# Kernel tuning notes

Measured on AMD Instinct MI355X. Metric: run time of the kernel, lower is better.

Reference implementation:

```python
import jax, jax.numpy as jnp
import numpy as np

N = 4096      # num_nodes
B = 32        # batch
U = 64        # num_units
L = 2         # num_rnn_layers
K = 2         # max_diffusion_step
OUT = 1       # output_dim (also decoder input_dim)
NM = 2 * K + 1  # num_matrices: 2 supports * K cheb steps + identity


def _random_walk_T(adj):
    # calculate_random_walk_matrix(adj).T : (D^-1 W)^T
    d = adj.sum(axis=1)
    return (adj / d[:, None]).T


def setup_inputs():
    key = jax.random.key(0)
    ks = jax.random.split(key, 16)
    adj = jax.random.uniform(ks[0], (N, N), dtype=jnp.float32)
    S_fwd = _random_walk_T(adj)      # forward transition, transposed
    S_bwd = _random_walk_T(adj.T)    # backward transition, transposed

    inputs = jax.random.normal(ks[1], (B, N, OUT), dtype=jnp.float32)
    hidden_state = jax.random.normal(ks[2], (L, B, N, U), dtype=jnp.float32) * 0.1

    D0 = OUT + U   # layer 0 gconv input width
    D1 = U + U     # layer 1 gconv input width
    s = 0.05
    Wg0 = jax.random.normal(ks[3], (NM * D0, 2 * U), jnp.float32) * s
    bg0 = jnp.ones((2 * U,), jnp.float32)          # bias_start = 1.0 for gates
    Wc0 = jax.random.normal(ks[4], (NM * D0, U), jnp.float32) * s
    bc0 = jnp.zeros((U,), jnp.float32)
    Wg1 = jax.random.normal(ks[5], (NM * D1, 2 * U), jnp.float32) * s
    bg1 = jnp.ones((2 * U,), jnp.float32)
    Wc1 = jax.random.normal(ks[6], (NM * D1, U), jnp.float32) * s
    bc1 = jnp.zeros((U,), jnp.float32)
    Wp = jax.random.normal(ks[7], (U, OUT), jnp.float32) * s
    bp = jnp.zeros((OUT,), jnp.float32)
    return {
        "inputs": inputs, "hidden_state": hidden_state,
        "S_fwd": S_fwd, "S_bwd": S_bwd,
        "Wg0": Wg0, "bg0": bg0, "Wc0": Wc0, "bc0": bc0,
        "Wg1": Wg1, "bg1": bg1, "Wc1": Wc1, "bc1": bc1,
        "Wp": Wp, "bp": bp,
    }


def _gconv(supports, x, h, W, b):
    # diffusion graph convolution with Chebyshev recursion (DCRNN)
    x0 = jnp.concatenate([x, h], axis=-1)      # (B, N, D)
    xs = [x0]
    for S in supports:
        x1 = jnp.einsum('mn,bnd->bmd', S, x0)
        xs.append(x1)
        xk_2, xk_1 = x0, x1
        for _ in range(K - 1):
            x2 = 2.0 * jnp.einsum('mn,bnd->bmd', S, xk_1) - xk_2
            xs.append(x2)
            xk_2, xk_1 = xk_1, x2
    X = jnp.concatenate(xs, axis=-1)           # (B, N, NM*D)
    return X @ W + b


def _dcgru_cell(supports, x, h, Wg, bg, Wc, bc):
    value = jax.nn.sigmoid(_gconv(supports, x, h, Wg, bg))   # (B, N, 2U)
    r, u = jnp.split(value, 2, axis=-1)
    c = jnp.tanh(_gconv(supports, x, r * h, Wc, bc))
    return u * h + (1.0 - u) * c


def reference(inputs, hidden_state, S_fwd, S_bwd,
              Wg0, bg0, Wc0, bc0, Wg1, bg1, Wc1, bc1, Wp, bp):
    supports = (S_fwd, S_bwd)
    layer_params = [(Wg0, bg0, Wc0, bc0), (Wg1, bg1, Wc1, bc1)]
    out = inputs
    new_hidden = []
    for i, (Wg, bg, Wc, bc) in enumerate(layer_params):
        h = _dcgru_cell(supports, out, hidden_state[i], Wg, bg, Wc, bc)
        new_hidden.append(h)
        out = h
    predict = out @ Wp + bp                    # (B, N, OUT)
    return predict, jnp.stack(new_hidden)
```

## Files before the change

kernel.cpp:

```cpp
#include <hip/hip_runtime.h>

typedef unsigned short u16;
typedef unsigned int u32;
typedef unsigned long long u64;
typedef short v8s __attribute__((ext_vector_type(8)));
typedef float v4f __attribute__((ext_vector_type(4)));

#define NN 4096
#define BATCH 32

__device__ __forceinline__ float b2f(u16 u) {
  union { u32 i; float f; } c; c.i = ((u32)u) << 16; return c.f;
}
__device__ __forceinline__ u16 f2b(float f) {
  union { float f; u32 i; } c; c.f = f;
  u32 x = c.i;
  return (u16)((x + 0x7fffu + ((x >> 16) & 1u)) >> 16);
}
__device__ __forceinline__ u32 pk2(float a, float b) {
  return (u32)f2b(a) | ((u32)f2b(b) << 16);
}

typedef const __attribute__((address_space(1))) u32* gp_t;
typedef __attribute__((address_space(3))) u32* lp_t;
__device__ __forceinline__ void gld16(const u16* g, u16* l) {
  __builtin_amdgcn_global_load_lds((gp_t)g, (lp_t)l, 16, 0, 0);
}

#define CBAR() asm volatile("" ::: "memory")
#define BARRIER() do { CBAR(); __builtin_amdgcn_s_barrier(); CBAR(); } while (0)
#define LGKM0() asm volatile("s_waitcnt lgkmcnt(0)" ::: "memory")
#define VMC4() asm volatile("s_waitcnt vmcnt(4)" ::: "memory")
#define VMC0() asm volatile("s_waitcnt vmcnt(0)" ::: "memory")

__global__ __launch_bounds__(256) void cvtS(const float* __restrict__ S,
                                            u16* __restrict__ Sb) {
  const u64 idx = ((u64)blockIdx.x * 256 + threadIdx.x) * 8;
  const float4 a = *(const float4*)(S + idx);
  const float4 b = *(const float4*)(S + idx + 4);
  uint4 o;
  o.x = pk2(a.x, a.y); o.y = pk2(a.z, a.w);
  o.z = pk2(b.x, b.y); o.w = pk2(b.z, b.w);
  *(uint4*)(Sb + idx) = o;
}

__global__ __launch_bounds__(512, 2) void gemm256(const u16* __restrict__ A,
                                                  const u16* __restrict__ B,
                                                  u16* __restrict__ Ct,
                                                  const u16* __restrict__ Xt) {
  __shared__ __align__(16) u16 lds[65536];
  const int t = threadIdx.x;
  const int wave = t >> 6, lane = t & 63;
  const int q = lane >> 4, r16 = lane & 15;
  const int wm = wave >> 2, wn = wave & 3;

  const int nwg = (int)(gridDim.x * gridDim.y);
  const int bid = (int)(blockIdx.y * gridDim.x + blockIdx.x);
  const int swz = (bid & 7) * (nwg >> 3) + (bid >> 3);
  const int m0 = (swz & 15) << 8;
  const int c0 = (swz >> 4) << 8;

  v4f acc[8][4];
  const v4f vz = {0.f, 0.f, 0.f, 0.f};
#pragma unroll
  for (int i = 0; i < 8; ++i)
#pragma unroll
    for (int j = 0; j < 4; ++j) acc[i][j] = vz;

  const int srow = t >> 3;
  const int sslot = ((t & 7) ^ (srow & 7)) << 3;
  const u16* pA = A + (u64)(m0 + srow) * NN + sslot;
  const u16* pB = B + (u64)(c0 + srow) * NN + sslot;
  const u64 rstep = (u64)64 * NN;
  const u64 hstep = (u64)128 * NN;
  u16* lw = lds + (wave << 9);

  const int sw8 = (q ^ (r16 & 7)) << 3;
  const int aBase = (wm << 13) + (r16 << 6) + sw8;
  const int bBase = 16384 + ((wn >> 1) << 13) + ((wn & 1) << 12) + (r16 << 6) + sw8;

  const int NT = NN >> 6;

  gld16(pA, lw);
  gld16(pA + rstep, lw + 4096);
  gld16(pA + hstep, lw + 8192);
  gld16(pA + hstep + rstep, lw + 12288);
  gld16(pB, lw + 16384);
  gld16(pB + rstep, lw + 20480);
  gld16(pB + hstep, lw + 24576);
  gld16(pB + hstep + rstep, lw + 28672);
  gld16(pB + 64, lw + 32768 + 16384);
  gld16(pB + 64 + rstep, lw + 32768 + 20480);
  gld16(pB + 64 + hstep, lw + 32768 + 24576);
  gld16(pB + 64 + hstep + rstep, lw + 32768 + 28672);
  VMC4();
  BARRIER();

#pragma unroll 2
  for (int T = 0; T < NT; ++T) {
    const int bo = (T & 1) << 15;
    const int no = bo ^ 32768;
    const u64 ka = (u64)(T + 1 < NT ? T + 1 : NT - 1) << 6;
    const u64 kb = (u64)(T + 2 < NT ? T + 2 : NT - 1) << 6;
    v8s af[4][2], bf[4][2];

#pragma unroll
    for (int i = 0; i < 4; ++i) {
      const int a = bo + aBase + (i << 10);
      af[i][0] = *(const v8s*)(lds + a);
      af[i][1] = *(const v8s*)(lds + (a ^ 32));
    }
#pragma unroll
    for (int j = 0; j < 2; ++j) {
      const int b = bo + bBase + (j << 10);
      bf[j][0] = *(const v8s*)(lds + b);
      bf[j][1] = *(const v8s*)(lds + (b ^ 32));
    }
    gld16(pA + ka, lw + no);
    gld16(pA + ka + rstep, lw + no + 4096);
    BARRIER();
    LGKM0();
    __builtin_amdgcn_s_setprio(1);
#pragma unroll
    for (int i = 0; i < 4; ++i)
#pragma unroll
      for (int j = 0; j < 2; ++j) {
        acc[i][j] = __builtin_amdgcn_mfma_f32_16x16x32_bf16(af[i][0], bf[j][0], acc[i][j], 0, 0, 0);
        acc[i][j] = __builtin_amdgcn_mfma_f32_16x16x32_bf16(af[i][1], bf[j][1], acc[i][j], 0, 0, 0);
      }
    __builtin_amdgcn_s_setprio(0);
    BARRIER();

#pragma unroll
    for (int j = 2; j < 4; ++j) {
      const int b = bo + bBase + (j << 10);
      bf[j][0] = *(const v8s*)(lds + b);
      bf[j][1] = *(const v8s*)(lds + (b ^ 32));
    }
    gld16(pA + hstep + ka, lw + no + 8192);
    gld16(pA + hstep + ka + rstep, lw + no + 12288);
    BARRIER();
    LGKM0();
    __builtin_amdgcn_s_setprio(1);
#pragma unroll
    for (int i = 0; i < 4; ++i)
#pragma unroll
      for (int j = 2; j < 4; ++j) {
        acc[i][j] = __builtin_amdgcn_mfma_f32_16x16x32_bf16(af[i][0], bf[j][0], acc[i][j], 0, 0, 0);
        acc[i][j] = __builtin_amdgcn_mfma_f32_16x16x32_bf16(af[i][1], bf[j][1], acc[i][j], 0, 0, 0);
      }
    __builtin_amdgcn_s_setprio(0);
    BARRIER();

#pragma unroll
    for (int i = 0; i < 4; ++i) {
      const int a = bo + aBase + ((4 + i) << 10);
      af[i][0] = *(const v8s*)(lds + a);
      af[i][1] = *(const v8s*)(lds + (a ^ 32));
    }
    gld16(pB + kb, lw + bo + 16384);
    gld16(pB + kb + rstep, lw + bo + 20480);
    BARRIER();
    LGKM0();
    __builtin_amdgcn_s_setprio(1);
#pragma unroll
    for (int i = 0; i < 4; ++i)
#pragma unroll
      for (int j = 2; j < 4; ++j) {
        acc[4 + i][j] = __builtin_amdgcn_mfma_f32_16x16x32_bf16(af[i][0], bf[j][0], acc[4 + i][j], 0, 0, 0);
        acc[4 + i][j] = __builtin_amdgcn_mfma_f32_16x16x32_bf16(af[i][1], bf[j][1], acc[4 + i][j], 0, 0, 0);
      }
    __builtin_amdgcn_s_setprio(0);
    BARRIER();

    gld16(pB + hstep + kb, lw + bo + 24576);
    gld16(pB + hstep + kb + rstep, lw + bo + 28672);
    BARRIER();
    __builtin_amdgcn_s_setprio(1);
#pragma unroll
    for (int i = 0; i < 4; ++i)
#pragma unroll
      for (int j = 0; j < 2; ++j) {
        acc[4 + i][j] = __builtin_amdgcn_mfma_f32_16x16x32_bf16(af[i][0], bf[j][0], acc[4 + i][j], 0, 0, 0);
        acc[4 + i][j] = __builtin_amdgcn_mfma_f32_16x16x32_bf16(af[i][1], bf[j][1], acc[4 + i][j], 0, 0, 0);
      }
    __builtin_amdgcn_s_setprio(0);
    VMC4();
    BARRIER();
  }

  VMC0();
  __syncthreads();
#pragma unroll
  for (int i = 0; i < 8; ++i)
#pragma unroll
    for (int j = 0; j < 4; ++j) {
      const int cl = (wn << 6) + (j << 4) + r16;
      const int ml = (wm << 7) + (i << 4) + (q << 2);
      const int phys = (cl << 8) + ((((ml >> 3) ^ (cl & 7)) << 3) | (ml & 7));
      uint2 pv;
      pv.x = pk2(acc[i][j][0], acc[i][j][1]);
      pv.y = pk2(acc[i][j][2], acc[i][j][3]);
      *(uint2*)(lds + phys) = pv;
    }
  __syncthreads();
#pragma unroll
  for (int it = 0; it < 16; ++it) {
    const int f = (it << 9) + t;
    const int cl = f >> 5, sl = f & 31;
    const int phys = (cl << 8) + ((sl ^ (cl & 7)) << 3);
    union { uint4 v; u16 e[8]; } tv;
    tv.v = *(const uint4*)(lds + phys);
    const u64 gi = (u64)(c0 + cl) * NN + m0 + (sl << 3);
    if (Xt) {
      union { uint4 v; u16 e[8]; } xv, ov;
      xv.v = *(const uint4*)(Xt + gi);
#pragma unroll
      for (int s = 0; s < 8; ++s) ov.e[s] = f2b(2.f * b2f(tv.e[s]) - b2f(xv.e[s]));
      *(uint4*)(Ct + gi) = ov.v;
    } else {
      *(uint4*)(Ct + gi) = tv.v;
    }
  }
}

__global__ __launch_bounds__(256) void gemm_s(const float* __restrict__ A,
                                              const u16* __restrict__ B,
                                              u16* __restrict__ Ct,
                                              const u16* __restrict__ Xt) {
  __shared__ __align__(16) u16 As[4096];
  __shared__ __align__(16) u16 Bs[4096];
  __shared__ __align__(16) u16 T[16384];
  const int t = threadIdx.x;
  const int wave = t >> 6, lane = t & 63;
  const int m0 = blockIdx.x << 7, c0 = blockIdx.y << 7;
  const int wm = (wave >> 1) << 6, wc = (wave & 1) << 6;
  const int q = lane >> 4, r16 = lane & 15;
  v4f acc[4][4];
  const v4f vz = {0.f, 0.f, 0.f, 0.f};
#pragma unroll
  for (int i = 0; i < 4; ++i)
#pragma unroll
    for (int j = 0; j < 4; ++j) acc[i][j] = vz;

  const int sr = t >> 2;
  const int sc = (t & 3) << 3;
  const u64 abase = (u64)(m0 + sr) * NN + sc;
  const u64 bbase = (u64)(c0 + sr) * NN + sc;
  const u64 rstep = (u64)64 * NN;
  u16* as0 = As + sr * 32 + sc;
  u16* as1 = As + (64 + sr) * 32 + sc;
  u16* bs0 = Bs + sr * 32 + sc;
  u16* bs1 = Bs + (64 + sr) * 32 + sc;

  for (int k0 = 0; k0 < NN; k0 += 32) {
    const float4 a0l = *(const float4*)(A + abase + k0);
    const float4 a0h = *(const float4*)(A + abase + k0 + 4);
    const float4 a1l = *(const float4*)(A + abase + rstep + k0);
    const float4 a1h = *(const float4*)(A + abase + rstep + k0 + 4);
    const uint4 b0 = *(const uint4*)(B + bbase + k0);
    const uint4 b1 = *(const uint4*)(B + bbase + rstep + k0);
    uint4 pa0, pa1;
    pa0.x = pk2(a0l.x, a0l.y); pa0.y = pk2(a0l.z, a0l.w);
    pa0.z = pk2(a0h.x, a0h.y); pa0.w = pk2(a0h.z, a0h.w);
    pa1.x = pk2(a1l.x, a1l.y); pa1.y = pk2(a1l.z, a1l.w);
    pa1.z = pk2(a1h.x, a1h.y); pa1.w = pk2(a1h.z, a1h.w);
    __syncthreads();
    *(uint4*)as0 = pa0;
    *(uint4*)as1 = pa1;
    *(uint4*)bs0 = b0;
    *(uint4*)bs1 = b1;
    __syncthreads();
    v8s af[4], bf[4];
#pragma unroll
    for (int i = 0; i < 4; ++i)
      af[i] = *(const v8s*)(As + ((wm + i * 16 + r16) << 5) + (q << 3));
#pragma unroll
    for (int j = 0; j < 4; ++j)
      bf[j] = *(const v8s*)(Bs + ((wc + j * 16 + r16) << 5) + (q << 3));
#pragma unroll
    for (int i = 0; i < 4; ++i)
#pragma unroll
      for (int j = 0; j < 4; ++j)
        acc[i][j] = __builtin_amdgcn_mfma_f32_16x16x32_bf16(af[i], bf[j], acc[i][j], 0, 0, 0);
  }
#pragma unroll
  for (int i = 0; i < 4; ++i)
#pragma unroll
    for (int j = 0; j < 4; ++j) {
      const int cl = wc + j * 16 + r16;
      const int mm = wm + i * 16 + (q << 2);
      uint2 pv;
      pv.x = pk2(acc[i][j][0], acc[i][j][1]);
      pv.y = pk2(acc[i][j][2], acc[i][j][3]);
      *(uint2*)(T + (cl << 7) + mm) = pv;
    }
  __syncthreads();
#pragma unroll
  for (int it = 0; it < 8; ++it) {
    const int flat = it * 256 + t;
    const int cl = flat >> 4;
    const int seg = (flat & 15) << 3;
    const u64 gi = (u64)(c0 + cl) * NN + m0 + seg;
    union { uint4 v; u16 e[8]; } tv;
    tv.v = *(uint4*)(T + (cl << 7) + seg);
    if (Xt) {
      union { uint4 v; u16 e[8]; } xv, ov;
      xv.v = *(const uint4*)(Xt + gi);
#pragma unroll
      for (int s = 0; s < 8; ++s) ov.e[s] = f2b(2.f * b2f(tv.e[s]) - b2f(xv.e[s]));
      *(uint4*)(Ct + gi) = ov.v;
    } else {
      *(uint4*)(Ct + gi) = tv.v;
    }
  }
}

template <int DP, int KTOT>
__global__ __launch_bounds__(256) void proj_k(const u16* __restrict__ Wt,
                                              const u16* __restrict__ F,
                                              const float* __restrict__ bias,
                                              u16* __restrict__ outp,
                                              const int JSTR, const int ACT) {
  __shared__ __align__(16) u16 As2[2048];
  __shared__ __align__(16) u16 Bs2[4096];
  const int t = threadIdx.x;
  const int wave = t >> 6, lane = t & 63;
  const int q = lane >> 4, r16 = lane & 15;
  const int n0 = blockIdx.x << 7;
  const int j0 = blockIdx.y << 6;
  const int b = blockIdx.z;
  v4f acc[4][2];
  const v4f vz = {0.f, 0.f, 0.f, 0.f};
#pragma unroll
  for (int i = 0; i < 4; ++i) { acc[i][0] = vz; acc[i][1] = vz; }

  const int ar = t >> 2, ac = (t & 3) << 3;
  const u64 wbase = (u64)(j0 + ar) * KTOT + ac;

  for (int k0 = 0; k0 < KTOT; k0 += 32) {
    const uint4 av = *(const uint4*)(Wt + wbase + k0);
    uint4 bv[2];
#pragma unroll
    for (int ci = 0; ci < 2; ++ci) {
      const int c = ci * 256 + t;
      const int kr = c >> 4;
      const int seg = (c & 15) << 3;
      const int kk = k0 + kr;
      const int i = kk / DP;
      const int d = kk - i * DP;
      bv[ci] = *(const uint4*)(F + ((u64)i * (BATCH * DP) + (u64)b * DP + d) * NN + n0 + seg);
    }
    __syncthreads();
    *(uint4*)(As2 + ar * 32 + ac) = av;
#pragma unroll
    for (int ci = 0; ci < 2; ++ci) {
      const int c = ci * 256 + t;
      const int kr = c >> 4;
      const int seg = (c & 15) << 3;
      *(uint4*)(Bs2 + (kr << 7) + seg) = bv[ci];
    }
    __syncthreads();
    v8s af[4], bf[2];
#pragma unroll
    for (int i = 0; i < 4; ++i)
      af[i] = *(const v8s*)(As2 + ((i * 16 + r16) << 5) + (q << 3));
#pragma unroll
    for (int jj = 0; jj < 2; ++jj) {
      const int nn = (wave << 5) + jj * 16 + r16;
      v8s v;
#pragma unroll
      for (int s = 0; s < 8; ++s) v[s] = (short)Bs2[(((q << 3) + s) << 7) + nn];
      bf[jj] = v;
    }
#pragma unroll
    for (int i = 0; i < 4; ++i)
#pragma unroll
      for (int jj = 0; jj < 2; ++jj)
        acc[i][jj] = __builtin_amdgcn_mfma_f32_16x16x32_bf16(af[i], bf[jj], acc[i][jj], 0, 0, 0);
  }
#pragma unroll
  for (int i = 0; i < 4; ++i)
#pragma unroll
    for (int jj = 0; jj < 2; ++jj)
#pragma unroll
      for (int r = 0; r < 4; ++r) {
        const int j = j0 + i * 16 + (q << 2) + r;
        const int n = n0 + (wave << 5) + jj * 16 + r16;
        float v = acc[i][jj][r] + bias[j];
        v = ACT ? (1.f - 2.f / (__expf(2.f * v) + 1.f)) : (1.f / (1.f + __expf(-v)));
        outp[((u64)b * JSTR + j) * NN + n] = f2b(v);
      }
}

__global__ __launch_bounds__(256) void repackW(const float* __restrict__ W, u16* __restrict__ Wt,
                                               const int D, const int DP, const int KTOT,
                                               const int J) {
  const int idx = blockIdx.x * 256 + threadIdx.x;
  if (idx >= J * KTOT) return;
  const int j = idx / KTOT, k = idx - j * KTOT;
  const int i = k / DP, d = k - i * DP;
  u16 v = 0;
  if (i < 5 && d < D) v = f2b(W[(i * D + d) * J + j]);
  Wt[idx] = v;
}

__global__ __launch_bounds__(256) void pack0(const float* __restrict__ x,
                                             const float* __restrict__ hid0,
                                             u16* __restrict__ F0) {
  __shared__ __align__(16) u16 Hs[64 * 72];
  const int b = blockIdx.y, n0 = blockIdx.x << 6, t = threadIdx.x;
  const int r = t >> 2, ds = t & 3;
  const float* hrow = hid0 + ((u64)b * NN + n0 + r) * 64;
#pragma unroll
  for (int c4 = 0; c4 < 4; ++c4) {
    const float4 v = *(const float4*)(hrow + ds * 16 + c4 * 4);
    uint2 p;
    p.x = pk2(v.x, v.y);
    p.y = pk2(v.z, v.w);
    *(uint2*)(Hs + r * 72 + ds * 16 + c4 * 4) = p;
  }
  __syncthreads();
#pragma unroll
  for (int c2 = 0; c2 < 2; ++c2) {
    union { uint4 v; u16 h[8]; } o;
#pragma unroll
    for (int s = 0; s < 8; ++s) o.h[s] = Hs[(ds * 16 + c2 * 8 + s) * 72 + r];
    *(uint4*)(F0 + ((u64)b * 72 + 1 + r) * NN + n0 + ds * 16 + c2 * 8) = o.v;
  }
  if (t < 64) {
    F0[(u64)b * 72 * NN + n0 + t] = f2b(x[(u64)b * NN + n0 + t]);
  } else if (t < 120) {
    const int tt = t - 64;
    const int row = 65 + (tt >> 3), seg = (tt & 7) << 3;
    uint4 z; z.x = z.y = z.z = z.w = 0;
    *(uint4*)(F0 + ((u64)b * 72 + row) * NN + n0 + seg) = z;
  }
}

__global__ __launch_bounds__(256) void pack1(const float* __restrict__ hid1,
                                             u16* __restrict__ F1) {
  __shared__ __align__(16) u16 Hs[64 * 72];
  const int b = blockIdx.y, n0 = blockIdx.x << 6, t = threadIdx.x;
  const int r = t >> 2, ds = t & 3;
  const float* hrow = hid1 + ((u64)b * NN + n0 + r) * 64;
#pragma unroll
  for (int c4 = 0; c4 < 4; ++c4) {
    const float4 v = *(const float4*)(hrow + ds * 16 + c4 * 4);
    uint2 p;
    p.x = pk2(v.x, v.y);
    p.y = pk2(v.z, v.w);
    *(uint2*)(Hs + r * 72 + ds * 16 + c4 * 4) = p;
  }
  __syncthreads();
#pragma unroll
  for (int c2 = 0; c2 < 2; ++c2) {
    union { uint4 v; u16 h[8]; } o;
#pragma unroll
    for (int s = 0; s < 8; ++s) o.h[s] = Hs[(ds * 16 + c2 * 8 + s) * 72 + r];
    *(uint4*)(F1 + ((u64)b * 128 + 64 + r) * NN + n0 + ds * 16 + c2 * 8) = o.v;
  }
}

__global__ __launch_bounds__(256) void candpack(const u16* __restrict__ G, u16* __restrict__ F,
                                                const int DP, const int OFF) {
  const int u = blockIdx.x * 256 + threadIdx.x;
  const int b = u >> 15;
  const int d = (u >> 9) & 63;
  const int seg = (u & 511) << 3;
  union { uint4 v; u16 h[8]; } g, f, o;
  g.v = *(const uint4*)(G + ((u64)b * 128 + d) * NN + seg);
  u16* fp = F + ((u64)b * DP + OFF + d) * NN + seg;
  f.v = *(const uint4*)fp;
#pragma unroll
  for (int s = 0; s < 8; ++s) o.h[s] = f2b(b2f(f.h[s]) * b2f(g.h[s]));
  *(uint4*)fp = o.v;
}

__global__ __launch_bounds__(256) void hnew_k(const u16* __restrict__ G,
                                              const float* __restrict__ hidL,
                                              u16* __restrict__ HnF,
                                              float* __restrict__ outH) {
  __shared__ __align__(16) float Hs[64 * 72];
  __shared__ __align__(16) float T2[64 * 72];
  const int b = blockIdx.y, n0 = blockIdx.x << 6, t = threadIdx.x;
  const int r = t >> 2, ds = t & 3;
  const float* hrow = hidL + ((u64)b * NN + n0 + r) * 64;
#pragma unroll
  for (int c4 = 0; c4 < 4; ++c4)
    *(float4*)(Hs + r * 72 + ds * 16 + c4 * 4) = *(const float4*)(hrow + ds * 16 + c4 * 4);
  __syncthreads();
#pragma unroll
  for (int c2 = 0; c2 < 2; ++c2) {
    const int ncol = ds * 16 + c2 * 8;
    union { uint4 v; u16 h[8]; } uv, cv, o;
    uv.v = *(const uint4*)(G + ((u64)b * 128 + 64 + r) * NN + n0 + ncol);
    cv.v = *(const uint4*)(G + ((u64)b * 128 + r) * NN + n0 + ncol);
#pragma unroll
    for (int s = 0; s < 8; ++s) {
      const int nl = ncol + s;
      const float uu = b2f(uv.h[s]);
      const float hh = Hs[nl * 72 + r];
      const float cc = b2f(cv.h[s]);
      const float v = uu * hh + (1.f - uu) * cc;
      o.h[s] = f2b(v);
      T2[nl * 72 + r] = v;
    }
    *(uint4*)(HnF + ((u64)b * 128 + r) * NN + n0 + ncol) = o.v;
  }
  __syncthreads();
  const int nl2 = t >> 2, dseg = (t & 3) << 4;
#pragma unroll
  for (int c4 = 0; c4 < 4; ++c4) {
    const float4 v = *(const float4*)(T2 + nl2 * 72 + dseg + c4 * 4);
    *(float4*)(outH + ((u64)b * NN + n0 + nl2) * 64 + dseg + c4 * 4) = v;
  }
}

__global__ __launch_bounds__(256) void predictk(const float* __restrict__ H1bnd,
                                                const float* __restrict__ Wp,
                                                const float* __restrict__ bp,
                                                float* __restrict__ outp) {
  __shared__ float w[64];
  __shared__ float bb;
  const int t = threadIdx.x;
  if (t < 64) w[t] = Wp[t];
  if (t == 64) bb = bp[0];
  __syncthreads();
  const int idx = blockIdx.x * 256 + t;
  const float* h = H1bnd + (u64)idx * 64;
  float acc = bb;
#pragma unroll
  for (int c4 = 0; c4 < 16; ++c4) {
    const float4 v = *(const float4*)(h + c4 * 4);
    acc += v.x * w[c4 * 4] + v.y * w[c4 * 4 + 1] + v.z * w[c4 * 4 + 2] + v.w * w[c4 * 4 + 3];
  }
  outp[idx] = acc;
}

static inline void launch_gemm(bool big, const float* Af, const u16* Ab,
                               const u16* B, u16* Ct, const u16* Xt,
                               int Cdim, hipStream_t s) {
  if (big) gemm256<<<dim3(16, Cdim >> 8), 512, 0, s>>>(Ab, B, Ct, Xt);
  else     gemm_s<<<dim3(32, Cdim >> 7), 256, 0, s>>>(Af, B, Ct, Xt);
}

extern "C" void kernel_launch(void* const* d_in, const int* in_sizes, int n_in,
                              void* d_out, int out_size, void* d_ws, size_t ws_size,
                              hipStream_t stream) {
  const float* X   = (const float*)d_in[0];
  const float* HID = (const float*)d_in[1];
  const float* Sf  = (const float*)d_in[2];
  const float* Sb  = (const float*)d_in[3];
  const float* Wg0 = (const float*)d_in[4];
  const float* bg0 = (const float*)d_in[5];
  const float* Wc0 = (const float*)d_in[6];
  const float* bc0 = (const float*)d_in[7];
  const float* Wg1 = (const float*)d_in[8];
  const float* bg1 = (const float*)d_in[9];
  const float* Wc1 = (const float*)d_in[10];
  const float* bc1 = (const float*)d_in[11];
  const float* Wp  = (const float*)d_in[12];
  const float* bp  = (const float*)d_in[13];
  float* OUT = (float*)d_out;
  char* ws = (char*)d_ws;

  u16* F = (u16*)(ws);
  u16* G = (u16*)(ws + 167772160ull);
  const u64 NEED_BIG = 167772160ull + 33554432ull + 2ull * 33554432ull + 393216ull;
  const bool big = ws_size >= NEED_BIG;
  u16* Sfb = (u16*)(ws + 167772160ull + 33554432ull);
  u16* Sbb = Sfb + (u64)NN * NN;
  u16* WT = big ? (Sbb + (u64)NN * NN)
                : (u16*)(ws + 167772160ull + 33554432ull);
  u16* Wg0t = WT;
  u16* Wc0t = Wg0t + 128 * 384;
  u16* Wg1t = Wc0t + 64 * 384;
  u16* Wc1t = Wg1t + 128 * 640;

  const float* HID1 = HID + (u64)32 * 4096 * 64;
  float* OUT_H0 = OUT + 131072;
  float* OUT_H1 = OUT + 131072 + 8388608;

  hipMemsetAsync(ws + (u64)11520 * NN * 2, 0, (u64)2304 * NN * 2, stream);

  if (big) {
    cvtS<<<8192, 256, 0, stream>>>(Sf, Sfb);
    cvtS<<<8192, 256, 0, stream>>>(Sb, Sbb);
  }

  repackW<<<(128 * 384 + 255) / 256, 256, 0, stream>>>(Wg0, Wg0t, 65, 72, 384, 128);
  repackW<<<(64 * 384 + 255) / 256, 256, 0, stream>>>(Wc0, Wc0t, 65, 72, 384, 64);
  repackW<<<(128 * 640 + 255) / 256, 256, 0, stream>>>(Wg1, Wg1t, 128, 128, 640, 128);
  repackW<<<(64 * 640 + 255) / 256, 256, 0, stream>>>(Wc1, Wc1t, 128, 128, 640, 64);

  pack0<<<dim3(64, 32), 256, 0, stream>>>(X, HID, F);
  const u64 R0 = (u64)2304 * NN;
  launch_gemm(big, Sf, Sfb, F, F + R0, nullptr, 2304, stream);
  launch_gemm(big, Sb, Sbb, F, F + 3 * R0, nullptr, 2304, stream);
  launch_gemm(big, Sf, Sfb, F + R0, F + 2 * R0, F, 2304, stream);
  launch_gemm(big, Sb, Sbb, F + 3 * R0, F + 4 * R0, F, 2304, stream);
  proj_k<72, 384><<<dim3(32, 2, 32), 256, 0, stream>>>(Wg0t, F, bg0, G, 128, 0);
  candpack<<<4096, 256, 0, stream>>>(G, F, 72, 1);
  launch_gemm(big, Sf, Sfb, F, F + R0, nullptr, 2304, stream);
  launch_gemm(big, Sb, Sbb, F, F + 3 * R0, nullptr, 2304, stream);
  launch_gemm(big, Sf, Sfb, F + R0, F + 2 * R0, F, 2304, stream);
  launch_gemm(big, Sb, Sbb, F + 3 * R0, F + 4 * R0, F, 2304, stream);
  proj_k<72, 384><<<dim3(32, 1, 32), 256, 0, stream>>>(Wc0t, F, bc0, G, 128, 1);
  hnew_k<<<dim3(64, 32), 256, 0, stream>>>(G, HID, F, OUT_H0);

  pack1<<<dim3(64, 32), 256, 0, stream>>>(HID1, F);
  const u64 R1 = (u64)4096 * NN;
  launch_gemm(big, Sf, Sfb, F, F + R1, nullptr, 4096, stream);
  launch_gemm(big, Sb, Sbb, F, F + 3 * R1, nullptr, 4096, stream);
  launch_gemm(big, Sf, Sfb, F + R1, F + 2 * R1, F, 4096, stream);
  launch_gemm(big, Sb, Sbb, F + 3 * R1, F + 4 * R1, F, 4096, stream);
  proj_k<128, 640><<<dim3(32, 2, 32), 256, 0, stream>>>(Wg1t, F, bg1, G, 128, 0);
  candpack<<<4096, 256, 0, stream>>>(G, F, 128, 64);
  launch_gemm(big, Sf, Sfb, F, F + R1, nullptr, 4096, stream);
  launch_gemm(big, Sb, Sbb, F, F + 3 * R1, nullptr, 4096, stream);
  launch_gemm(big, Sf, Sfb, F + R1, F + 2 * R1, F, 4096, stream);
  launch_gemm(big, Sb, Sbb, F + 3 * R1, F + 4 * R1, F, 4096, stream);
  proj_k<128, 640><<<dim3(32, 1, 32), 256, 0, stream>>>(Wc1t, F, bc1, G, 128, 1);
  hnew_k<<<dim3(64, 32), 256, 0, stream>>>(G, HID1, F, OUT_H1);

  predictk<<<512, 256, 0, stream>>>(OUT_H1, Wp, bp, OUT);
}
```

Baseline: 2.206 ms.

## Restructure big GEMM to 16 waves with 256x192 variant for layer 0

The 256x256 bf16 GEMM moves from 8 waves to 16 waves (1024 threads). Each wave now owns a 64x64 sub-tile with 16 accumulators, and the four-phase main loop becomes two phases with fewer barriers. A new 256x192 tile kernel is added for layer 0, whose feature width is 2304, so the grid is 16x12 instead of 16x9 with 256-wide tiles. The aim is more latency hiding per CU, lower register pressure per wave and better CU fill for layer 0, at the cost of less operand reuse per wave and a heavier barrier with more waves.

After: 1.901 ms. 13.8% less time.

```diff
diff --git a/kernel.cpp b/kernel.cpp
--- a/kernel.cpp
+++ b/kernel.cpp
@@ -30,7 +30,7 @@
 #define CBAR() asm volatile("" ::: "memory")
 #define BARRIER() do { CBAR(); __builtin_amdgcn_s_barrier(); CBAR(); } while (0)
 #define LGKM0() asm volatile("s_waitcnt lgkmcnt(0)" ::: "memory")
-#define VMC4() asm volatile("s_waitcnt vmcnt(4)" ::: "memory")
+#define VMC2() asm volatile("s_waitcnt vmcnt(2)" ::: "memory")
 #define VMC0() asm volatile("s_waitcnt vmcnt(0)" ::: "memory")
 
 __global__ __launch_bounds__(256) void cvtS(const float* __restrict__ S,
@@ -44,10 +44,10 @@
   *(uint4*)(Sb + idx) = o;
 }
 
-__global__ __launch_bounds__(512, 2) void gemm256(const u16* __restrict__ A,
-                                                  const u16* __restrict__ B,
-                                                  u16* __restrict__ Ct,
-                                                  const u16* __restrict__ Xt) {
+__global__ __launch_bounds__(1024, 4) void gemm256(const u16* __restrict__ A,
+                                                   const u16* __restrict__ B,
+                                                   u16* __restrict__ Ct,
+                                                   const u16* __restrict__ Xt) {
   __shared__ __align__(16) u16 lds[65536];
   const int t = threadIdx.x;
   const int wave = t >> 6, lane = t & 63;
@@ -60,10 +60,10 @@
   const int m0 = (swz & 15) << 8;
   const int c0 = (swz >> 4) << 8;
 
-  v4f acc[8][4];
+  v4f acc[4][4];
   const v4f vz = {0.f, 0.f, 0.f, 0.f};
 #pragma unroll
-  for (int i = 0; i < 8; ++i)
+  for (int i = 0; i < 4; ++i)
 #pragma unroll
     for (int j = 0; j < 4; ++j) acc[i][j] = vz;
 
@@ -71,29 +71,22 @@
   const int sslot = ((t & 7) ^ (srow & 7)) << 3;
   const u16* pA = A + (u64)(m0 + srow) * NN + sslot;
   const u16* pB = B + (u64)(c0 + srow) * NN + sslot;
-  const u64 rstep = (u64)64 * NN;
-  const u64 hstep = (u64)128 * NN;
+  const u64 rstep = (u64)128 * NN;
   u16* lw = lds + (wave << 9);
 
   const int sw8 = (q ^ (r16 & 7)) << 3;
-  const int aBase = (wm << 13) + (r16 << 6) + sw8;
-  const int bBase = 16384 + ((wn >> 1) << 13) + ((wn & 1) << 12) + (r16 << 6) + sw8;
+  const int aBase = (wm << 12) + (r16 << 6) + sw8;
+  const int bBase = 16384 + (wn << 12) + (r16 << 6) + sw8;
 
   const int NT = NN >> 6;
 
   gld16(pA, lw);
-  gld16(pA + rstep, lw + 4096);
-  gld16(pA + hstep, lw + 8192);
-  gld16(pA + hstep + rstep, lw + 12288);
+  gld16(pA + rstep, lw + 8192);
   gld16(pB, lw + 16384);
-  gld16(pB + rstep, lw + 20480);
-  gld16(pB + hstep, lw + 24576);
-  gld16(pB + hstep + rstep, lw + 28672);
+  gld16(pB + rstep, lw + 24576);
   gld16(pB + 64, lw + 32768 + 16384);
-  gld16(pB + 64 + rstep, lw + 32768 + 20480);
-  gld16(pB + 64 + hstep, lw + 32768 + 24576);
-  gld16(pB + 64 + hstep + rstep, lw + 32768 + 28672);
-  VMC4();
+  gld16(pB + 64 + rstep, lw + 32768 + 24576);
+  VMC2();
   BARRIER();
 
 #pragma unroll 2
@@ -102,101 +95,54 @@
     const int no = bo ^ 32768;
     const u64 ka = (u64)(T + 1 < NT ? T + 1 : NT - 1) << 6;
     const u64 kb = (u64)(T + 2 < NT ? T + 2 : NT - 1) << 6;
-    v8s af[4][2], bf[4][2];
-
-#pragma unroll
-    for (int i = 0; i < 4; ++i) {
-      const int a = bo + aBase + (i << 10);
-      af[i][0] = *(const v8s*)(lds + a);
-      af[i][1] = *(const v8s*)(lds + (a ^ 32));
-    }
-#pragma unroll
-    for (int j = 0; j < 2; ++j) {
-      const int b = bo + bBase + (j << 10);
-      bf[j][0] = *(const v8s*)(lds + b);
-      bf[j][1] = *(const v8s*)(lds + (b ^ 32));
-    }
+
     gld16(pA + ka, lw + no);
-    gld16(pA + ka + rstep, lw + no + 4096);
+    gld16(pA + ka + rstep, lw + no + 8192);
+    {
+      v8s af[4], bf[4];
+#pragma unroll
+      for (int i = 0; i < 4; ++i) af[i] = *(const v8s*)(lds + bo + aBase + (i << 10));
+#pragma unroll
+      for (int j = 0; j < 4; ++j) bf[j] = *(const v8s*)(lds + bo + bBase + (j << 10));
+      __builtin_amdgcn_s_setprio(1);
+#pragma unroll
+      for (int i = 0; i < 4; ++i)
+#pragma unroll
+        for (int j = 0; j < 4; ++j)
+          acc[i][j] = __builtin_amdgcn_mfma_f32_16x16x32_bf16(af[i], bf[j], acc[i][j], 0, 0, 0);
+      __builtin_amdgcn_s_setprio(0);
+    }
+
+    {
+      v8s ag[4], bg[4];
+#pragma unroll
+      for (int i = 0; i < 4; ++i) ag[i] = *(const v8s*)(lds + ((bo + aBase + (i << 10)) ^ 32));
+#pragma unroll
+      for (int j = 0; j < 4; ++j) bg[j] = *(const v8s*)(lds + ((bo + bBase + (j << 10)) ^ 32));
+      LGKM0();
+      BARRIER();
+      gld16(pB + kb, lw + bo + 16384);
+      gld16(pB + kb + rstep, lw + bo + 24576);
+      __builtin_amdgcn_s_setprio(1);
+#pragma unroll
+      for (int i = 0; i < 4; ++i)
+#pragma unroll
+        for (int j = 0; j < 4; ++j)
+          acc[i][j] = __builtin_amdgcn_mfma_f32_16x16x32_bf16(ag[i], bg[j], acc[i][j], 0, 0, 0);
+      __builtin_amdgcn_s_setprio(0);
+    }
+    VMC2();
     BARRIER();
-    LGKM0();
-    __builtin_amdgcn_s_setprio(1);
-#pragma unroll
-    for (int i = 0; i < 4; ++i)
-#pragma unroll
-      for (int j = 0; j < 2; ++j) {
-        acc[i][j] = __builtin_amdgcn_mfma_f32_16x16x32_bf16(af[i][0], bf[j][0], acc[i][j], 0, 0, 0);
-        acc[i][j] = __builtin_amdgcn_mfma_f32_16x16x32_bf16(af[i][1], bf[j][1], acc[i][j], 0, 0, 0);
-      }
-    __builtin_amdgcn_s_setprio(0);
-    BARRIER();
-
-#pragma unroll
-    for (int j = 2; j < 4; ++j) {
-      const int b = bo + bBase + (j << 10);
-      bf[j][0] = *(const v8s*)(lds + b);
-      bf[j][1] = *(const v8s*)(lds + (b ^ 32));
-    }
-    gld16(pA + hstep + ka, lw + no + 8192);
-    gld16(pA + hstep + ka + rstep, lw + no + 12288);
-    BARRIER();
-    LGKM0();
-    __builtin_amdgcn_s_setprio(1);
-#pragma unroll
-    for (int i = 0; i < 4; ++i)
-#pragma unroll
-      for (int j = 2; j < 4; ++j) {
-        acc[i][j] = __builtin_amdgcn_mfma_f32_16x16x32_bf16(af[i][0], bf[j][0], acc[i][j], 0, 0, 0);
-        acc[i][j] = __builtin_amdgcn_mfma_f32_16x16x32_bf16(af[i][1], bf[j][1], acc[i][j], 0, 0, 0);
-      }
-    __builtin_amdgcn_s_setprio(0);
-    BARRIER();
-
-#pragma unroll
-    for (int i = 0; i < 4; ++i) {
-      const int a = bo + aBase + ((4 + i) << 10);
-      af[i][0] = *(const v8s*)(lds + a);
-      af[i][1] = *(const v8s*)(lds + (a ^ 32));
-    }
-    gld16(pB + kb, lw + bo + 16384);
-    gld16(pB + kb + rstep, lw + bo + 20480);
-    BARRIER();
-    LGKM0();
-    __builtin_amdgcn_s_setprio(1);
-#pragma unroll
-    for (int i = 0; i < 4; ++i)
-#pragma unroll
-      for (int j = 2; j < 4; ++j) {
-        acc[4 + i][j] = __builtin_amdgcn_mfma_f32_16x16x32_bf16(af[i][0], bf[j][0], acc[4 + i][j], 0, 0, 0);
-        acc[4 + i][j] = __builtin_amdgcn_mfma_f32_16x16x32_bf16(af[i][1], bf[j][1], acc[4 + i][j], 0, 0, 0);
-      }
-    __builtin_amdgcn_s_setprio(0);
-    BARRIER();
-
-    gld16(pB + hstep + kb, lw + bo + 24576);
-    gld16(pB + hstep + kb + rstep, lw + bo + 28672);
-    BARRIER();
-    __builtin_amdgcn_s_setprio(1);
-#pragma unroll
-    for (int i = 0; i < 4; ++i)
-#pragma unroll
-      for (int j = 0; j < 2; ++j) {
-        acc[4 + i][j] = __builtin_amdgcn_mfma_f32_16x16x32_bf16(af[i][0], bf[j][0], acc[4 + i][j], 0, 0, 0);
-        acc[4 + i][j] = __builtin_amdgcn_mfma_f32_16x16x32_bf16(af[i][1], bf[j][1], acc[4 + i][j], 0, 0, 0);
-      }
-    __builtin_amdgcn_s_setprio(0);
-    VMC4();
-    BARRIER();
   }
 
   VMC0();
   __syncthreads();
 #pragma unroll
-  for (int i = 0; i < 8; ++i)
+  for (int i = 0; i < 4; ++i)
 #pragma unroll
     for (int j = 0; j < 4; ++j) {
       const int cl = (wn << 6) + (j << 4) + r16;
-      const int ml = (wm << 7) + (i << 4) + (q << 2);
+      const int ml = (wm << 6) + (i << 4) + (q << 2);
       const int phys = (cl << 8) + ((((ml >> 3) ^ (cl & 7)) << 3) | (ml & 7));
       uint2 pv;
       pv.x = pk2(acc[i][j][0], acc[i][j][1]);
@@ -205,8 +151,134 @@
     }
   __syncthreads();
 #pragma unroll
-  for (int it = 0; it < 16; ++it) {
-    const int f = (it << 9) + t;
+  for (int it = 0; it < 8; ++it) {
+    const int f = (it << 10) + t;
+    const int cl = f >> 5, sl = f & 31;
+    const int phys = (cl << 8) + ((sl ^ (cl & 7)) << 3);
+    union { uint4 v; u16 e[8]; } tv;
+    tv.v = *(const uint4*)(lds + phys);
+    const u64 gi = (u64)(c0 + cl) * NN + m0 + (sl << 3);
+    if (Xt) {
+      union { uint4 v; u16 e[8]; } xv, ov;
+      xv.v = *(const uint4*)(Xt + gi);
+#pragma unroll
+      for (int s = 0; s < 8; ++s) ov.e[s] = f2b(2.f * b2f(tv.e[s]) - b2f(xv.e[s]));
+      *(uint4*)(Ct + gi) = ov.v;
+    } else {
+      *(uint4*)(Ct + gi) = tv.v;
+    }
+  }
+}
+
+__global__ __launch_bounds__(1024, 4) void gemm192(const u16* __restrict__ A,
+                                                   const u16* __restrict__ B,
+                                                   u16* __restrict__ Ct,
+                                                   const u16* __restrict__ Xt) {
+  __shared__ __align__(16) u16 lds[65536];
+  const int t = threadIdx.x;
+  const int wave = t >> 6, lane = t & 63;
+  const int q = lane >> 4, r16 = lane & 15;
+  const int wm = wave >> 2, wn = wave & 3;
+
+  const int nwg = (int)(gridDim.x * gridDim.y);
+  const int bid = (int)(blockIdx.y * gridDim.x + blockIdx.x);
+  const int swz = (bid & 7) * (nwg >> 3) + (bid >> 3);
+  const int m0 = (swz & 15) << 8;
+  const int c0 = (swz >> 4) * 192;
+
+  v4f acc[4][3];
+  const v4f vz = {0.f, 0.f, 0.f, 0.f};
+#pragma unroll
+  for (int i = 0; i < 4; ++i)
+#pragma unroll
+    for (int j = 0; j < 3; ++j) acc[i][j] = vz;
+
+  const int srow = t >> 3;
+  const int sslot = ((t & 7) ^ (srow & 7)) << 3;
+  const u16* pA = A + (u64)(m0 + srow) * NN + sslot;
+  const u16* pB = B + (u64)(c0 + srow) * NN + sslot;
+  const u64 rstep = (u64)128 * NN;
+  u16* lw = lds + (wave << 9);
+
+  const int sw8 = (q ^ (r16 & 7)) << 3;
+  const int aBase = (wm << 12) + (r16 << 6) + sw8;
+  const int bBase = 16384 + wn * 3072 + (r16 << 6) + sw8;
+
+  const int NT = NN >> 6;
+
+  gld16(pA, lw);
+  gld16(pA + rstep, lw + 8192);
+  gld16(pB, lw + 16384);
+  gld16(pB + rstep, lw + 24576);
+  gld16(pB + 64, lw + 32768 + 16384);
+  gld16(pB + 64 + rstep, lw + 32768 + 24576);
+  VMC2();
+  BARRIER();
+
+#pragma unroll 2
+  for (int T = 0; T < NT; ++T) {
+    const int bo = (T & 1) << 15;
+    const int no = bo ^ 32768;
+    const u64 ka = (u64)(T + 1 < NT ? T + 1 : NT - 1) << 6;
+    const u64 kb = (u64)(T + 2 < NT ? T + 2 : NT - 1) << 6;
+
+    gld16(pA + ka, lw + no);
+    gld16(pA + ka + rstep, lw + no + 8192);
+    {
+      v8s af[4], bf[3];
+#pragma unroll
+      for (int i = 0; i < 4; ++i) af[i] = *(const v8s*)(lds + bo + aBase + (i << 10));
+#pragma unroll
+      for (int j = 0; j < 3; ++j) bf[j] = *(const v8s*)(lds + bo + bBase + (j << 10));
+      __builtin_amdgcn_s_setprio(1);
+#pragma unroll
+      for (int i = 0; i < 4; ++i)
+#pragma unroll
+        for (int j = 0; j < 3; ++j)
+          acc[i][j] = __builtin_amdgcn_mfma_f32_16x16x32_bf16(af[i], bf[j], acc[i][j], 0, 0, 0);
+      __builtin_amdgcn_s_setprio(0);
+    }
+
+    {
+      v8s ag[4], bg[3];
+#pragma unroll
+      for (int i = 0; i < 4; ++i) ag[i] = *(const v8s*)(lds + ((bo + aBase + (i << 10)) ^ 32));
+#pragma unroll
+      for (int j = 0; j < 3; ++j) bg[j] = *(const v8s*)(lds + ((bo + bBase + (j << 10)) ^ 32));
+      LGKM0();
+      BARRIER();
+      gld16(pB + kb, lw + bo + 16384);
+      gld16(pB + kb + rstep, lw + bo + 24576);
+      __builtin_amdgcn_s_setprio(1);
+#pragma unroll
+      for (int i = 0; i < 4; ++i)
+#pragma unroll
+        for (int j = 0; j < 3; ++j)
+          acc[i][j] = __builtin_amdgcn_mfma_f32_16x16x32_bf16(ag[i], bg[j], acc[i][j], 0, 0, 0);
+      __builtin_amdgcn_s_setprio(0);
+    }
+    VMC2();
+    BARRIER();
+  }
+
+  VMC0();
+  __syncthreads();
+#pragma unroll
+  for (int i = 0; i < 4; ++i)
+#pragma unroll
+    for (int j = 0; j < 3; ++j) {
+      const int cl = wn * 48 + (j << 4) + r16;
+      const int ml = (wm << 6) + (i << 4) + (q << 2);
+      const int phys = (cl << 8) + ((((ml >> 3) ^ (cl & 7)) << 3) | (ml & 7));
+      uint2 pv;
+      pv.x = pk2(acc[i][j][0], acc[i][j][1]);
+      pv.y = pk2(acc[i][j][2], acc[i][j][3]);
+      *(uint2*)(lds + phys) = pv;
+    }
+  __syncthreads();
+#pragma unroll
+  for (int it = 0; it < 6; ++it) {
+    const int f = (it << 10) + t;
     const int cl = f >> 5, sl = f & 31;
     const int phys = (cl << 8) + ((sl ^ (cl & 7)) << 3);
     union { uint4 v; u16 e[8]; } tv;
@@ -538,13 +610,6 @@
   outp[idx] = acc;
 }
 
-static inline void launch_gemm(bool big, const float* Af, const u16* Ab,
-                               const u16* B, u16* Ct, const u16* Xt,
-                               int Cdim, hipStream_t s) {
-  if (big) gemm256<<<dim3(16, Cdim >> 8), 512, 0, s>>>(Ab, B, Ct, Xt);
-  else     gemm_s<<<dim3(32, Cdim >> 7), 256, 0, s>>>(Af, B, Ct, Xt);
-}
-
 extern "C" void kernel_launch(void* const* d_in, const int* in_sizes, int n_in,
                               void* d_out, int out_size, void* d_ws, size_t ws_size,
                               hipStream_t stream) {
@@ -596,31 +661,61 @@
 
   pack0<<<dim3(64, 32), 256, 0, stream>>>(X, HID, F);
   const u64 R0 = (u64)2304 * NN;
-  launch_gemm(big, Sf, Sfb, F, F + R0, nullptr, 2304, stream);
-  launch_gemm(big, Sb, Sbb, F, F + 3 * R0, nullptr, 2304, stream);
-  launch_gemm(big, Sf, Sfb, F + R0, F + 2 * R0, F, 2304, stream);
-  launch_gemm(big, Sb, Sbb, F + 3 * R0, F + 4 * R0, F, 2304, stream);
+  const dim3 g192(16, 12);
+  if (big) {
+    gemm192<<<g192, 1024, 0, stream>>>(Sfb, F, F + R0, nullptr);
+    gemm192<<<g192, 1024, 0, stream>>>(Sbb, F, F + 3 * R0, nullptr);
+    gemm192<<<g192, 1024, 0, stream>>>(Sfb, F + R0, F + 2 * R0, F);
+    gemm192<<<g192, 1024, 0, stream>>>(Sbb, F + 3 * R0, F + 4 * R0, F);
+  } else {
+    gemm_s<<<dim3(32, 18), 256, 0, stream>>>(Sf, F, F + R0, nullptr);
+    gemm_s<<<dim3(32, 18), 256, 0, stream>>>(Sb, F, F + 3 * R0, nullptr);
+    gemm_s<<<dim3(32, 18), 256, 0, stream>>>(Sf, F + R0, F + 2 * R0, F);
+    gemm_s<<<dim3(32, 18), 256, 0, stream>>>(Sb, F + 3 * R0, F + 4 * R0, F);
+  }
   proj_k<72, 384><<<dim3(32, 2, 32), 256, 0, stream>>>(Wg0t, F, bg0, G, 128, 0);
   candpack<<<4096, 256, 0, stream>>>(G, F, 72, 1);
-  launch_gemm(big, Sf, Sfb, F, F + R0, nullptr, 2304, stream);
-  launch_gemm(big, Sb, Sbb, F, F + 3 * R0, nullptr, 2304, stream);
-  launch_gemm(big, Sf, Sfb, F + R0, F + 2 * R0, F, 2304, stream);
-  launch_gemm(big, Sb, Sbb, F + 3 * R0, F + 4 * R0, F, 2304, stream);
+  if (big) {
+    gemm192<<<g192, 1024, 0, stream>>>(Sfb, F, F + R0, nullptr);
+    gemm192<<<g192, 1024, 0, stream>>>(Sbb, F, F + 3 * R0, nullptr);
+    gemm192<<<g192, 1024, 0, stream>>>(Sfb, F + R0, F + 2 * R0, F);
+    gemm192<<<g192, 1024, 0, stream>>>(Sbb, F + 3 * R0, F + 4 * R0, F);
+  } else {
+    gemm_s<<<dim3(32, 18), 256, 0, stream>>>(Sf, F, F + R0, nullptr);
+    gemm_s<<<dim3(32, 18), 256, 0, stream>>>(Sb, F, F + 3 * R0, nullptr);
+    gemm_s<<<dim3(32, 18), 256, 0, stream>>>(Sf, F + R0, F + 2 * R0, F);
+    gemm_s<<<dim3(32, 18), 256, 0, stream>>>(Sb, F + 3 * R0, F + 4 * R0, F);
+  }
   proj_k<72, 384><<<dim3(32, 1, 32), 256, 0, stream>>>(Wc0t, F, bc0, G, 128, 1);
   hnew_k<<<dim3(64, 32), 256, 0, stream>>>(G, HID, F, OUT_H0);
 
   pack1<<<dim3(64, 32), 256, 0, stream>>>(HID1, F);
   const u64 R1 = (u64)4096 * NN;
-  launch_gemm(big, Sf, Sfb, F, F + R1, nullptr, 4096, stream);
-  launch_gemm(big, Sb, Sbb, F, F + 3 * R1, nullptr, 4096, stream);
-  launch_gemm(big, Sf, Sfb, F + R1, F + 2 * R1, F, 4096, stream);
-  launch_gemm(big, Sb, Sbb, F + 3 * R1, F + 4 * R1, F, 4096, stream);
+  const dim3 g256(16, 16);
+  if (big) {
+    gemm256<<<g256, 1024, 0, stream>>>(Sfb, F, F + R1, nullptr);
+    gemm256<<<g256, 1024, 0, stream>>>(Sbb, F, F + 3 * R1, nullptr);
+    gemm256<<<g256, 1024, 0, stream>>>(Sfb, F + R1, F + 2 * R1, F);
+    gemm256<<<g256, 1024, 0, stream>>>(Sbb, F + 3 * R1, F + 4 * R1, F);
+  } else {
+    gemm_s<<<dim3(32, 32), 256, 0, stream>>>(Sf, F, F + R1, nullptr);
+    gemm_s<<<dim3(32, 32), 256, 0, stream>>>(Sb, F, F + 3 * R1, nullptr);
+    gemm_s<<<dim3(32, 32), 256, 0, stream>>>(Sf, F + R1, F + 2 * R1, F);
+    gemm_s<<<dim3(32, 32), 256, 0, stream>>>(Sb, F + 3 * R1, F + 4 * R1, F);
+  }
   proj_k<128, 640><<<dim3(32, 2, 32), 256, 0, stream>>>(Wg1t, F, bg1, G, 128, 0);
   candpack<<<4096, 256, 0, stream>>>(G, F, 128, 64);
-  launch_gemm(big, Sf, Sfb, F, F + R1, nullptr, 4096, stream);
-  launch_gemm(big, Sb, Sbb, F, F + 3 * R1, nullptr, 4096, stream);
-  launch_gemm(big, Sf, Sfb, F + R1, F + 2 * R1, F, 4096, stream);
-  launch_gemm(big, Sb, Sbb, F + 3 * R1, F + 4 * R1, F, 4096, stream);
+  if (big) {
+    gemm256<<<g256, 1024, 0, stream>>>(Sfb, F, F + R1, nullptr);
+    gemm256<<<g256, 1024, 0, stream>>>(Sbb, F, F + 3 * R1, nullptr);
+    gemm256<<<g256, 1024, 0, stream>>>(Sfb, F + R1, F + 2 * R1, F);
+    gemm256<<<g256, 1024, 0, stream>>>(Sbb, F + 3 * R1, F + 4 * R1, F);
+  } else {
+    gemm_s<<<dim3(32, 32), 256, 0, stream>>>(Sf, F, F + R1, nullptr);
+    gemm_s<<<dim3(32, 32), 256, 0, stream>>>(Sb, F, F + 3 * R1, nullptr);
+    gemm_s<<<dim3(32, 32), 256, 0, stream>>>(Sf, F + R1, F + 2 * R1, F);
+    gemm_s<<<dim3(32, 32), 256, 0, stream>>>(Sb, F + 3 * R1, F + 4 * R1, F);
+  }
   proj_k<128, 640><<<dim3(32, 1, 32), 256, 0, stream>>>(Wc1t, F, bc1, G, 128, 1);
   hnew_k<<<dim3(64, 32), 256, 0, stream>>>(G, HID1, F, OUT_H1);
 
```
